# Kernel optimization log

Hardware: AMD Instinct MI355X
Metric: run time of the kernel (lower is better)

The kernel has to match this reference:

```python
import jax, jax.numpy as jnp
import numpy as np

LN_EPS = 1e-5
RMS_EPS = 1e-5

B, T, D = 4, 2048, 1024
H, DK, DV = 4, 256, 512            # head_k_dim = D/H, head_v_dim = expand_v * head_k_dim (expand_v=2)
KDIM, VDIM = H * DK, H * DV        # 1024, 2048
FFN = 4096                          # int(d_model * ffn_ratio)
CONV = 4


def _layernorm(x, w, b):
    mu = jnp.mean(x, -1, keepdims=True)
    var = jnp.mean(jnp.square(x - mu), -1, keepdims=True)
    return (x - mu) * jax.lax.rsqrt(var + LN_EPS) * w + b


def _short_conv_silu(x, w):
    # causal depthwise conv, kernel size K, then SiLU. x: [B,T,C], w: [C,K]
    K = w.shape[1]
    xp = jnp.pad(x, ((0, 0), (K - 1, 0), (0, 0)))
    y = sum(xp[:, i:i + x.shape[1], :] * w[:, i] for i in range(K))
    return jax.nn.silu(y)


def _l2norm(x):
    return x * jax.lax.rsqrt(jnp.sum(jnp.square(x), -1, keepdims=True) + 1e-6)


def _gated_delta_rule(q, k, v, g, beta):
    # q,k: [B,T,H,DK]; v: [B,T,H,DV]; g,beta: [B,T,H]
    # S_t = exp(g_t)*S_{t-1} + k_t (beta_t*(v_t - k_t^T exp(g_t) S_{t-1}))^T ; o_t = q_t^T S_t
    def step(S, inp):
        qt, kt, vt, gt, bt = inp
        S = S * jnp.exp(gt)[..., None, None]          # [B,H,DK,DV]
        mem = jnp.einsum('bhk,bhkv->bhv', kt, S)
        delta = (vt - mem) * bt[..., None]
        S = S + jnp.einsum('bhk,bhv->bhkv', kt, delta)
        o = jnp.einsum('bhk,bhkv->bhv', qt, S)
        return S, o
    S0 = jnp.zeros((q.shape[0], H, DK, DV), q.dtype)
    xs = (q.transpose(1, 0, 2, 3), k.transpose(1, 0, 2, 3), v.transpose(1, 0, 2, 3),
          g.transpose(1, 0, 2), beta.transpose(1, 0, 2))
    _, o = jax.lax.scan(step, S0, xs)
    return o.transpose(1, 0, 2, 3)  # [B,T,H,DV]


def setup_inputs() -> dict:
    key = jax.random.key(0)
    ks = jax.random.split(key, 24)
    n = lambda k, shp, s=0.02: jax.random.normal(k, shp, dtype=jnp.float32) * s
    return {
        'x': jax.random.normal(ks[0], (B, T, D), dtype=jnp.float32),
        'Wq': n(ks[1], (D, KDIM)), 'Wk': n(ks[2], (D, KDIM)), 'Wv': n(ks[3], (D, VDIM)),
        'Wa': n(ks[4], (D, H)), 'Wb': n(ks[5], (D, H)), 'Wg': n(ks[6], (D, VDIM)),
        'conv_q_w': n(ks[7], (KDIM, CONV), 0.2), 'conv_k_w': n(ks[8], (KDIM, CONV), 0.2),
        'conv_v_w': n(ks[9], (VDIM, CONV), 0.2),
        'A_log': jnp.log(jax.random.uniform(ks[10], (H,), minval=1.0, maxval=16.0, dtype=jnp.float32)),
        'dt_bias': jax.random.uniform(ks[11], (H,), minval=0.0, maxval=0.5, dtype=jnp.float32),
        'o_norm_w': jnp.ones((DV,), jnp.float32),
        'Wo': n(ks[12], (VDIM, D)),
        'ln1_w': jnp.ones((D,), jnp.float32), 'ln1_b': jnp.zeros((D,), jnp.float32),
        'ln2_w': jnp.ones((D,), jnp.float32), 'ln2_b': jnp.zeros((D,), jnp.float32),
        'ffn_w1': n(ks[13], (D, FFN)), 'ffn_b1': jnp.zeros((FFN,), jnp.float32),
        'ffn_w2': n(ks[14], (FFN, D)), 'ffn_b2': jnp.zeros((D,), jnp.float32),
    }


def reference(x, Wq, Wk, Wv, Wa, Wb, Wg, conv_q_w, conv_k_w, conv_v_w, A_log, dt_bias,
              o_norm_w, Wo, ln1_w, ln1_b, ln2_w, ln2_b, ffn_w1, ffn_b1, ffn_w2, ffn_b2):
    normed = _layernorm(x, ln1_w, ln1_b)
    q = _short_conv_silu(normed @ Wq, conv_q_w).reshape(B, T, H, DK)
    k = _short_conv_silu(normed @ Wk, conv_k_w).reshape(B, T, H, DK)
    v = _short_conv_silu(normed @ Wv, conv_v_w).reshape(B, T, H, DV)
    q = _l2norm(q) * (DK ** -0.5)
    k = _l2norm(k)
    g = -jnp.exp(A_log) * jax.nn.softplus(normed @ Wa + dt_bias)   # [B,T,H], negative
    beta = jax.nn.sigmoid(normed @ Wb)                              # [B,T,H]
    o = _gated_delta_rule(q, k, v, g, beta)                         # [B,T,H,DV]
    gate = (normed @ Wg).reshape(B, T, H, DV)
    o = o * jax.lax.rsqrt(jnp.mean(jnp.square(o), -1, keepdims=True) + RMS_EPS)
    o = o * o_norm_w * jax.nn.silu(gate)                            # gated RMSNorm
    x = x + o.reshape(B, T, VDIM) @ Wo
    h = _layernorm(x, ln2_w, ln2_b)
    ffn = jax.nn.gelu(h @ ffn_w1 + ffn_b1, approximate=False) @ ffn_w2 + ffn_b2
    return x + ffn
```

## Files before the change

kernel.cpp:

```cpp
#include <hip/hip_runtime.h>
#include <math.h>

#define B_    4
#define T_    2048
#define D_    1024
#define H_    4
#define DK_   256
#define DV_   512
#define KDIM_ 1024
#define VDIM_ 2048
#define FFN_  4096
#define BT_   8192

typedef unsigned short bf16;
typedef __attribute__((ext_vector_type(8))) short short8;
typedef __attribute__((ext_vector_type(4))) short short4v;
typedef __attribute__((ext_vector_type(4))) float f32x4;


__device__ __forceinline__ float sigmoidf_(float x) { return 1.f / (1.f + expf(-x)); }
__device__ __forceinline__ float siluf_(float x)    { return x / (1.f + expf(-x)); }
__device__ __forceinline__ float geluf_(float x)    { return 0.5f * x * (1.f + erff(x * 0.70710678118654752f)); }

__device__ __forceinline__ float bf2f(bf16 u) {
  union { unsigned int i; float f; } c; c.i = (unsigned int)u << 16; return c.f;
}
__device__ __forceinline__ bf16 f2bf(float f) {
  union { unsigned int i; float f; } c; c.f = f;
  unsigned int r = c.i + 0x7fffu + ((c.i >> 16) & 1u);
  return (bf16)(r >> 16);
}

__device__ __forceinline__ void gload16(const bf16* g, bf16* l) {
  __builtin_amdgcn_global_load_lds((__attribute__((address_space(1))) const void*)g,
                                   (__attribute__((address_space(3))) void*)l, 16, 0, 0);
}

__device__ __forceinline__ void storeC(float* p, float v) { *p = v; }
__device__ __forceinline__ void storeC(bf16* p, float v)  { *p = f2bf(v); }

__device__ __forceinline__ short8 ld76(const bf16* p) {
  union { short8 v; short4v h[2]; } u;
  u.h[0] = *(const short4v*)p;
  u.h[1] = *(const short4v*)(p + 4);
  return u.v;
}
__device__ __forceinline__ void st4bf(bf16* p, f32x4 v) {
  short4v o;
  o[0] = (short)f2bf(v[0]); o[1] = (short)f2bf(v[1]);
  o[2] = (short)f2bf(v[2]); o[3] = (short)f2bf(v[3]);
  *(short4v*)p = o;
}

__device__ __forceinline__ float block_sum256(float v, float* red) {
#pragma unroll
  for (int off = 32; off; off >>= 1) v += __shfl_xor(v, off, 64);
  __syncthreads();
  if ((threadIdx.x & 63) == 0) red[threadIdx.x >> 6] = v;
  __syncthreads();
  return red[0] + red[1] + red[2] + red[3];
}


__global__ __launch_bounds__(256) void sentinel_kernel(float* out, int n) {
  int i = blockIdx.x * 256 + threadIdx.x;
  if (i < n) out[i] = 12345.0f;
}


__global__ __launch_bounds__(256) void ln_kernel(const float* __restrict__ x,
                                                 const float* __restrict__ w,
                                                 const float* __restrict__ b,
                                                 bf16* __restrict__ y) {
  __shared__ float red[4];
  int row = blockIdx.x;
  const float* xr = x + (size_t)row * D_;
  float xv[4];
  float s = 0.f;
#pragma unroll
  for (int i = 0; i < 4; i++) { xv[i] = xr[threadIdx.x + 256 * i]; s += xv[i]; }
  float mean = block_sum256(s, red) * (1.f / D_);
  float s2 = 0.f;
#pragma unroll
  for (int i = 0; i < 4; i++) { float d = xv[i] - mean; s2 += d * d; }
  float var = block_sum256(s2, red) * (1.f / D_);
  float inv = rsqrtf(var + 1e-5f);
  bf16* yr = y + (size_t)row * D_;
#pragma unroll
  for (int i = 0; i < 4; i++) {
    int c = threadIdx.x + 256 * i;
    yr[c] = f2bf((xv[i] - mean) * inv * w[c] + b[c]);
  }
}


__global__ __launch_bounds__(256) void convT_kernel(const float* __restrict__ src,
                                                    bf16* __restrict__ dst,
                                                    int K, int N) {
  __shared__ float t[32][33];
  int n0 = blockIdx.x * 32, k0 = blockIdx.y * 32;
  int tx = threadIdx.x & 31, ty = threadIdx.x >> 5;
#pragma unroll
  for (int i = 0; i < 4; i++)
    t[ty + i * 8][tx] = src[(size_t)(k0 + ty + i * 8) * N + n0 + tx];
  __syncthreads();
#pragma unroll
  for (int i = 0; i < 4; i++)
    dst[(size_t)(n0 + ty + i * 8) * K + k0 + tx] = f2bf(t[tx][ty + i * 8]);
}


__global__ __launch_bounds__(256) void kT_kernel(const bf16* __restrict__ k16,
                                                 bf16* __restrict__ kT) {
  __shared__ bf16 tile[32][34];
  int t0 = blockIdx.x * 32;
  int d0 = blockIdx.y * 32;
  int bh = blockIdx.z;
  int b = bh >> 2, h = bh & 3;
  int tx = threadIdx.x & 31, ty = threadIdx.x >> 5;
#pragma unroll
  for (int i = 0; i < 4; i++)
    tile[ty + 8 * i][tx] = k16[(size_t)(b * T_ + t0 + ty + 8 * i) * KDIM_ + h * DK_ + d0 + tx];
  __syncthreads();
#pragma unroll
  for (int i = 0; i < 4; i++)
    kT[((size_t)bh * DK_ + d0 + ty + 8 * i) * T_ + t0 + tx] = tile[tx][ty + 8 * i];
}


template <typename TC>
__global__ __launch_bounds__(256) void gemm_mfma(const bf16* __restrict__ A,
                                                 const bf16* __restrict__ Bt,
                                                 const float* __restrict__ bias,
                                                 const float* __restrict__ res,
                                                 TC* __restrict__ C,
                                                 int N, int K, int flags) {
  __shared__ __align__(16) bf16 As[128 * 32];
  __shared__ __align__(16) bf16 Bs[128 * 32];
  int tid = threadIdx.x;
  int wave = tid >> 6, lane = tid & 63;
  int bm = blockIdx.y * 128, bn = blockIdx.x * 128;
  int wm = (wave >> 1) * 64, wn = (wave & 1) * 64;
  int lm = lane & 15;
  int quad = lane >> 4;

  f32x4 acc[4][4];
#pragma unroll
  for (int i = 0; i < 4; i++)
#pragma unroll
    for (int j = 0; j < 4; j++) acc[i][j] = (f32x4){0.f, 0.f, 0.f, 0.f};

  int srow = wave * 32 + (lane >> 2);
  int scol = (lane & 3) * 8;
  const bf16* ag = A  + (size_t)(bm + srow) * K + scol;
  const bf16* bg = Bt + (size_t)(bn + srow) * K + scol;
  bf16* al = As + wave * 32 * 32;
  bf16* bl = Bs + wave * 32 * 32;
  const size_t gstep = (size_t)16 * K;

  for (int k0 = 0; k0 < K; k0 += 32) {
    gload16(ag + k0,         al);
    gload16(ag + k0 + gstep, al + 16 * 32);
    gload16(bg + k0,         bl);
    gload16(bg + k0 + gstep, bl + 16 * 32);
    __syncthreads();

    short8 af[4], bf[4];
#pragma unroll
    for (int i = 0; i < 4; i++)
      af[i] = *(const short8*)&As[(wm + i * 16 + lm) * 32 + quad * 8];
#pragma unroll
    for (int j = 0; j < 4; j++)
      bf[j] = *(const short8*)&Bs[(wn + j * 16 + lm) * 32 + quad * 8];
#pragma unroll
    for (int i = 0; i < 4; i++)
#pragma unroll
      for (int j = 0; j < 4; j++)
        acc[i][j] = __builtin_amdgcn_mfma_f32_16x16x32_bf16(af[i], bf[j], acc[i][j], 0, 0, 0);
    __syncthreads();
  }

#pragma unroll
  for (int i = 0; i < 4; i++) {
    int row0 = bm + wm + i * 16 + quad * 4;
#pragma unroll
    for (int j = 0; j < 4; j++) {
      int col = bn + wn + j * 16 + lm;
      float badd = (flags & 1) ? bias[col] : 0.f;
#pragma unroll
      for (int r = 0; r < 4; r++) {
        float v = acc[i][j][r] + badd;
        if (flags & 2) v = geluf_(v);
        if (flags & 4) v += res[(size_t)(row0 + r) * N + col];
        storeC(&C[(size_t)(row0 + r) * N + col], v);
      }
    }
  }
}


__global__ __launch_bounds__(256) void ab_kernel(const bf16* __restrict__ normed,
                                                 const float* __restrict__ Wa,
                                                 const float* __restrict__ Wb,
                                                 const float* __restrict__ A_log,
                                                 const float* __restrict__ dt_bias,
                                                 float* __restrict__ g,
                                                 float* __restrict__ beta) {
  __shared__ float red[4];
  int row = blockIdx.x;
  const bf16* xr = normed + (size_t)row * D_;
  float aacc[4] = {}, bacc[4] = {};
#pragma unroll
  for (int i = 0; i < 4; i++) {
    int d = threadIdx.x + 256 * i;
    float xv = bf2f(xr[d]);
    float4 wa = *(const float4*)&Wa[d * 4];
    float4 wb = *(const float4*)&Wb[d * 4];
    aacc[0] += xv * wa.x; aacc[1] += xv * wa.y; aacc[2] += xv * wa.z; aacc[3] += xv * wa.w;
    bacc[0] += xv * wb.x; bacc[1] += xv * wb.y; bacc[2] += xv * wb.z; bacc[3] += xv * wb.w;
  }
  float sa[4], sb[4];
#pragma unroll
  for (int h = 0; h < 4; h++) {
    sa[h] = block_sum256(aacc[h], red);
    sb[h] = block_sum256(bacc[h], red);
  }
  if (threadIdx.x < 4) {
    int h = threadIdx.x;
    float xa = sa[h] + dt_bias[h];
    float sp = (xa > 20.f) ? xa : log1pf(expf(xa));
    g[row * 4 + h] = -expf(A_log[h]) * sp;
    beta[row * 4 + h] = sigmoidf_(sb[h]);
  }
}


__global__ __launch_bounds__(256) void conv_qk_kernel(const float* __restrict__ pre,
                                                      const float* __restrict__ convw,
                                                      bf16* __restrict__ out,
                                                      float scale) {
  __shared__ float red[4];
  int blk = blockIdx.x;
  int h = blk & 3;
  int bt = blk >> 2;
  int t = bt & (T_ - 1);
  int c = h * DK_ + threadIdx.x;
  float y = 0.f;
#pragma unroll
  for (int i = 0; i < 4; i++) {
    int tt = t + i - 3;
    if (tt >= 0) y += pre[(size_t)(bt + i - 3) * KDIM_ + c] * convw[c * 4 + i];
  }
  y = siluf_(y);
  float ss = block_sum256(y * y, red);
  y *= rsqrtf(ss + 1e-6f) * scale;
  out[(size_t)bt * KDIM_ + c] = f2bf(y);
}

__global__ __launch_bounds__(256) void conv_v_kernel(const float* __restrict__ pre,
                                                     const float* __restrict__ convw,
                                                     bf16* __restrict__ out) {
  int idx = blockIdx.x * 256 + threadIdx.x;
  int c = idx & (VDIM_ - 1);
  int bt = idx >> 11;
  int t = bt & (T_ - 1);
  float y = 0.f;
#pragma unroll
  for (int i = 0; i < 4; i++) {
    int tt = t + i - 3;
    if (tt >= 0) y += pre[(size_t)(bt + i - 3) * VDIM_ + c] * convw[c * 4 + i];
  }
  out[idx] = f2bf(siluf_(y));
}


#define SP 76

__global__ __launch_bounds__(256, 2) void delta_p1(const bf16* __restrict__ q,
                                                   const bf16* __restrict__ k,
                                                   const bf16* __restrict__ v,
                                                   const float* __restrict__ g,
                                                   const float* __restrict__ beta,
                                                   bf16* __restrict__ Pg,
                                                   bf16* __restrict__ Wg,
                                                   bf16* __restrict__ Yg,
                                                   float* __restrict__ gsc) {
  __shared__ bf16 Abf[64 * SP];
  __shared__ bf16 DTg[64 * SP];
  __shared__ float Ub[64 * 64];
  __shared__ float Gc[64], Lm[64], Bt[64];

  int blk = blockIdx.x;
  int c = blk & 31, bh = blk >> 5;
  int b = bh >> 2, h = bh & 3;
  int tid = threadIdx.x;
  int wave = tid >> 6, lane = tid & 63;
  int lm = lane & 15, quad = lane >> 4;
  int r0 = c * 64;

  const bf16* kb = k + (size_t)b * T_ * KDIM_ + h * DK_;
  const bf16* qb = q + (size_t)b * T_ * KDIM_ + h * DK_;
  const bf16* vb = v + (size_t)b * T_ * VDIM_ + h * DV_;
  const float* gbp = g    + (size_t)b * T_ * H_ + h;
  const float* bbp = beta + (size_t)b * T_ * H_ + h;
  size_t cb = (size_t)bh * 32 + c;
  bf16* PgC = Pg + cb * 4096;
  bf16* WgC = Wg + cb * 64 * 512;
  bf16* YgC = Yg + cb * 64 * 256;

  if (wave == 0) {
    float gv = gbp[(size_t)(r0 + lane) * H_];
    float bv = bbp[(size_t)(r0 + lane) * H_];
#pragma unroll
    for (int d = 1; d < 64; d <<= 1) {
      float nn = __shfl_up(gv, (unsigned)d, 64);
      if (lane >= d) gv += nn;
    }
    Gc[lane] = gv; Lm[lane] = expf(gv); Bt[lane] = bv;
    gsc[cb * 64 + lane] = gv;
  }
  __syncthreads();

  {
    f32x4 akk[4], aqk[4];
#pragma unroll
    for (int j = 0; j < 4; j++) { akk[j] = (f32x4){0.f,0.f,0.f,0.f}; aqk[j] = (f32x4){0.f,0.f,0.f,0.f}; }
    const bf16* krow = kb + (size_t)(r0 + 16 * wave + lm) * KDIM_;
    const bf16* qrow = qb + (size_t)(r0 + 16 * wave + lm) * KDIM_;
#pragma unroll
    for (int ks = 0; ks < 8; ks++) {
      short8 ak = *(const short8*)(krow + 8 * quad + 32 * ks);
      short8 aq = *(const short8*)(qrow + 8 * quad + 32 * ks);
#pragma unroll
      for (int j = 0; j < 4; j++) {
        short8 bk = *(const short8*)(kb + (size_t)(r0 + 16 * j + lm) * KDIM_ + 8 * quad + 32 * ks);
        akk[j] = __builtin_amdgcn_mfma_f32_16x16x32_bf16(ak, bk, akk[j], 0, 0, 0);
        aqk[j] = __builtin_amdgcn_mfma_f32_16x16x32_bf16(aq, bk, aqk[j], 0, 0, 0);
      }
    }
    float gi[4], bi[4];
#pragma unroll
    for (int r = 0; r < 4; r++) {
      int i = 16 * wave + 4 * quad + r;
      gi[r] = Gc[i]; bi[r] = Bt[i];
    }
#pragma unroll
    for (int j = 0; j < 4; j++) {
      int s = 16 * j + lm;
      float gs = Gc[s];
#pragma unroll
      for (int r = 0; r < 4; r++) {
        int i = 16 * wave + 4 * quad + r;
        float dec = expf(gi[r] - gs);
        Abf[(size_t)i * SP + s] = f2bf((s < i)  ? bi[r] * dec * akk[j][r] : 0.f);
        PgC[(size_t)i * 64 + s] = f2bf((s <= i) ? dec * aqk[j][r]        : 0.f);
      }
    }
  }

  for (int grp = 0; grp < 12; grp++) {
    __syncthreads();
    {
      int* dz = (int*)DTg;
#pragma unroll
      for (int i = 0; i < 10; i++) {
        int idx = tid + 256 * i;
        if (idx < 64 * SP / 2) dz[idx] = 0;
      }
    }
    int cg = 16 * wave + lm;
#pragma unroll
    for (int ti = 0; ti < 4; ti++)
#pragma unroll
      for (int r = 0; r < 4; r++) {
        int t = 16 * ti + 4 * quad + r;
        float val;
        if (grp < 8) val = Bt[t] * bf2f(vb[(size_t)(r0 + t) * VDIM_ + grp * 64 + cg]);
        else         val = Bt[t] * Lm[t] * bf2f(kb[(size_t)(r0 + t) * KDIM_ + (grp - 8) * 64 + cg]);
        Ub[t * 64 + cg] = val;
      }
    __syncthreads();

#pragma unroll
    for (int j = 0; j < 4; j++) {
      if (j > 0) {
        f32x4 racc = (f32x4){0.f, 0.f, 0.f, 0.f};
        int nk = (j == 3) ? 2 : 1;
        for (int ks = 0; ks < nk; ks++) {
          short8 aa = ld76(&Abf[(size_t)(16 * j + lm) * SP + 8 * quad + 32 * ks]);
          short8 bd = ld76(&DTg[(size_t)(16 * wave + lm) * SP + 8 * quad + 32 * ks]);
          racc = __builtin_amdgcn_mfma_f32_16x16x32_bf16(aa, bd, racc, 0, 0, 0);
        }
#pragma unroll
        for (int r = 0; r < 4; r++)
          Ub[(16 * j + 4 * quad + r) * 64 + 16 * wave + lm] -= racc[r];
        __syncthreads();
      }
      if (wave == 0) {
        int tl = lane & 15, sg = lane >> 4;
        short4v ab4 = *(const short4v*)&Abf[(size_t)(16 * j + tl) * SP + 16 * j + 4 * sg];
        float av[4];
        av[0] = bf2f((bf16)ab4[0]); av[1] = bf2f((bf16)ab4[1]);
        av[2] = bf2f((bf16)ab4[2]); av[3] = bf2f((bf16)ab4[3]);
        float d[16];
#pragma unroll
        for (int t = 0; t < 16; t++) {
          float val = Ub[(16 * j + t) * 64 + lane];
#pragma unroll
          for (int s = 0; s < t; s++) {
            float ats = __shfl(av[s & 3], t + 16 * (s >> 2), 64);
            val -= ats * d[s];
          }
          d[t] = val;
          DTg[(size_t)lane * SP + 16 * j + t] = f2bf(val);
        }
      }
      __syncthreads();
    }

#pragma unroll
    for (int ti = 0; ti < 4; ti++)
#pragma unroll
      for (int r = 0; r < 4; r++) {
        int t = 16 * ti + 4 * quad + r;
        bf16 val = DTg[(size_t)(16 * wave + lm) * SP + t];
        if (grp < 8) WgC[(size_t)t * 512 + grp * 64 + cg] = val;
        else         YgC[(size_t)t * 256 + (grp - 8) * 64 + cg] = val;
      }
  }
}


#define SP2 264
#define SD  72

__global__ __launch_bounds__(256, 1) void delta_p2(const bf16* __restrict__ q,
                                                   const bf16* __restrict__ kT,
                                                   const bf16* __restrict__ Wg,
                                                   const bf16* __restrict__ Yg,
                                                   const bf16* __restrict__ Pg,
                                                   const float* __restrict__ gsc,
                                                   bf16* __restrict__ o) {
  __shared__ bf16 ST[32 * SP2];
  __shared__ bf16 dT[32 * SD];
  __shared__ bf16 dTe[32 * SD];
  __shared__ float Gc[64];
  __shared__ __align__(16) bf16 Ks[8 * 256 * 8];

  int blk = blockIdx.x;
  int vs = blk & 15, bh = blk >> 4;
  int b = bh >> 2, h = bh & 3;
  int tid = threadIdx.x;
  int wave = tid >> 6, lane = tid & 63;
  int lm = lane & 15, quad = lane >> 4;
  int r2 = wave >> 1, ct = wave & 1;
  int v0 = vs * 32;

  const bf16* qb  = q  + (size_t)b * T_ * KDIM_ + h * DK_;
  const bf16* kTb = kT + (size_t)bh * DK_ * T_;
  bf16*       ob  = o  + (size_t)b * T_ * VDIM_ + h * DV_ + v0;

  f32x4 Sacc[8];
#pragma unroll
  for (int i = 0; i < 8; i++) Sacc[i] = (f32x4){0.f, 0.f, 0.f, 0.f};

  float gnext = gsc[(size_t)bh * 32 * 64 + lane];
  short8 qfr[2][8], yfr[2][8];
  {
    const bf16* yc0 = Yg + (size_t)bh * 32 * 64 * 256;
#pragma unroll
    for (int i = 0; i < 2; i++) {
      const bf16* qrow = qb + (size_t)(16 * (2 * r2 + i) + lm) * KDIM_;
      const bf16* yrow = yc0 + (size_t)(16 * (2 * r2 + i) + lm) * 256;
#pragma unroll
      for (int kf = 0; kf < 8; kf++) {
        qfr[i][kf] = *(const short8*)(qrow + 8 * quad + 32 * kf);
        yfr[i][kf] = *(const short8*)(yrow + 8 * quad + 32 * kf);
      }
    }
  }

  for (int c = 0; c < 32; c++) {
    const int r0 = c * 64;
    const size_t cb = (size_t)bh * 32 + c;

#pragma unroll
    for (int i = 0; i < 8; i++)
      gload16(kTb + (size_t)tid * T_ + r0 + i * 8, Ks + i * 2048 + wave * 512);
    __builtin_amdgcn_sched_barrier(0);

    const bf16* pc = Pg + cb * 4096;
    short8 pfr[2][2];
#pragma unroll
    for (int i = 0; i < 2; i++)
#pragma unroll
      for (int kf = 0; kf < 2; kf++)
        pfr[i][kf] = *(const short8*)(pc + (size_t)(16 * (2 * r2 + i) + lm) * 64 + 8 * quad + 32 * kf);

    const bf16* wcp = Wg + cb * 64 * 512 + v0 + 16 * ct + lm;
    bf16 wfr[2][4];
#pragma unroll
    for (int i = 0; i < 2; i++)
#pragma unroll
      for (int rr = 0; rr < 4; rr++)
        wfr[i][rr] = wcp[(size_t)(16 * (2 * r2 + i) + 4 * quad + rr) * 512];
    __builtin_amdgcn_sched_barrier(0);

#pragma unroll
    for (int di = 0; di < 8; di++)
      st4bf(&ST[(size_t)(16 * ct + lm) * SP2 + 16 * (8 * r2 + di) + 4 * quad], Sacc[di]);
    Gc[lane] = gnext;
    asm volatile("s_waitcnt lgkmcnt(0)" ::: "memory");
    __builtin_amdgcn_s_barrier();

    short8 Bs[8];
#pragma unroll
    for (int kf = 0; kf < 8; kf++)
      Bs[kf] = *(const short8*)&ST[(size_t)(16 * ct + lm) * SP2 + 8 * quad + 32 * kf];

    f32x4 Yacc[2], Oacc[2];
#pragma unroll
    for (int i = 0; i < 2; i++) { Yacc[i] = (f32x4){0.f,0.f,0.f,0.f}; Oacc[i] = (f32x4){0.f,0.f,0.f,0.f}; }
#pragma unroll
    for (int i = 0; i < 2; i++)
#pragma unroll
      for (int kf = 0; kf < 8; kf++) {
        Yacc[i] = __builtin_amdgcn_mfma_f32_16x16x32_bf16(yfr[i][kf], Bs[kf], Yacc[i], 0, 0, 0);
        Oacc[i] = __builtin_amdgcn_mfma_f32_16x16x32_bf16(qfr[i][kf], Bs[kf], Oacc[i], 0, 0, 0);
      }

    __builtin_amdgcn_sched_barrier(0);
    {
      int cn = (c + 1) & 31;
      size_t cbn = (size_t)bh * 32 + cn;
      int rn = cn * 64;
      gnext = gsc[cbn * 64 + lane];
      const bf16* ycn = Yg + cbn * 64 * 256;
#pragma unroll
      for (int i = 0; i < 2; i++) {
        const bf16* qrow = qb + (size_t)(rn + 16 * (2 * r2 + i) + lm) * KDIM_;
        const bf16* yrow = ycn + (size_t)(16 * (2 * r2 + i) + lm) * 256;
#pragma unroll
        for (int kf = 0; kf < 8; kf++) {
          qfr[i][kf] = *(const short8*)(qrow + 8 * quad + 32 * kf);
          yfr[i][kf] = *(const short8*)(yrow + 8 * quad + 32 * kf);
        }
      }
    }
    __builtin_amdgcn_sched_barrier(0);

    float g63 = Gc[63];
#pragma unroll
    for (int i = 0; i < 2; i++) {
      int rt = 2 * r2 + i;
#pragma unroll
      for (int rr = 0; rr < 4; rr++) {
        int row = 16 * rt + 4 * quad + rr;
        float gr  = Gc[row];
        float lam = expf(gr);
        float er  = expf(g63 - gr);
        float dv = bf2f(wfr[i][rr]) - Yacc[i][rr];
        Oacc[i][rr] *= lam;
        dT [(size_t)(16 * ct + lm) * SD + row] = f2bf(dv);
        dTe[(size_t)(16 * ct + lm) * SD + row] = f2bf(dv * er);
      }
    }
    asm volatile("s_waitcnt lgkmcnt(0)" ::: "memory");
    __builtin_amdgcn_s_barrier();

#pragma unroll
    for (int i = 0; i < 2; i++) {
#pragma unroll
      for (int kf = 0; kf < 2; kf++) {
        short8 bd = *(const short8*)&dT[(size_t)(16 * ct + lm) * SD + 8 * quad + 32 * kf];
        Oacc[i] = __builtin_amdgcn_mfma_f32_16x16x32_bf16(pfr[i][kf], bd, Oacc[i], 0, 0, 0);
      }
#pragma unroll
      for (int rr = 0; rr < 4; rr++) {
        int row = 16 * (2 * r2 + i) + 4 * quad + rr;
        ob[(size_t)(r0 + row) * VDIM_ + 16 * ct + lm] = f2bf(Oacc[i][rr]);
      }
    }

    float lend = expf(g63);
    short8 Be[2];
#pragma unroll
    for (int kf = 0; kf < 2; kf++)
      Be[kf] = *(const short8*)&dTe[(size_t)(16 * ct + lm) * SD + 8 * quad + 32 * kf];
#pragma unroll
    for (int di = 0; di < 8; di++) {
      int D = 8 * r2 + di;
      f32x4 s = Sacc[di];
      s[0] *= lend; s[1] *= lend; s[2] *= lend; s[3] *= lend;
#pragma unroll
      for (int kf = 0; kf < 2; kf++) {
        short8 ka = *(const short8*)&Ks[((size_t)(quad + 4 * kf) * 256 + 16 * D + lm) * 8];
        s = __builtin_amdgcn_mfma_f32_16x16x32_bf16(ka, Be[kf], s, 0, 0, 0);
      }
      Sacc[di] = s;
    }
    asm volatile("s_waitcnt lgkmcnt(0)" ::: "memory");
    __builtin_amdgcn_s_barrier();
  }
}


__global__ __launch_bounds__(256) void gated_rms_kernel(bf16* __restrict__ o,
                                                        const bf16* __restrict__ gate,
                                                        const float* __restrict__ onw) {
  __shared__ float red[4];
  int blk = blockIdx.x;
  int h = blk & 3;
  int bt = blk >> 2;
  size_t base = (size_t)bt * VDIM_ + h * DV_;
  int tid = threadIdx.x;
  float o1 = bf2f(o[base + tid]), o2 = bf2f(o[base + tid + 256]);
  float ss = block_sum256(o1 * o1 + o2 * o2, red);
  float s = rsqrtf(ss * (1.f / DV_) + 1e-5f);
  float g1 = bf2f(gate[base + tid]), g2 = bf2f(gate[base + tid + 256]);
  o[base + tid]       = f2bf(o1 * s * onw[tid] * siluf_(g1));
  o[base + tid + 256] = f2bf(o2 * s * onw[tid + 256] * siluf_(g2));
}


extern "C" void kernel_launch(void* const* d_in, const int* in_sizes, int n_in,
                              void* d_out, int out_size, void* d_ws, size_t ws_size,
                              hipStream_t stream) {
  const float* x        = (const float*)d_in[0];
  const float* Wq       = (const float*)d_in[1];
  const float* Wk       = (const float*)d_in[2];
  const float* Wv       = (const float*)d_in[3];
  const float* Wa       = (const float*)d_in[4];
  const float* Wb       = (const float*)d_in[5];
  const float* Wg       = (const float*)d_in[6];
  const float* conv_q_w = (const float*)d_in[7];
  const float* conv_k_w = (const float*)d_in[8];
  const float* conv_v_w = (const float*)d_in[9];
  const float* A_log    = (const float*)d_in[10];
  const float* dt_bias  = (const float*)d_in[11];
  const float* o_norm_w = (const float*)d_in[12];
  const float* Wo       = (const float*)d_in[13];
  const float* ln1_w    = (const float*)d_in[14];
  const float* ln1_b    = (const float*)d_in[15];
  const float* ln2_w    = (const float*)d_in[16];
  const float* ln2_b    = (const float*)d_in[17];
  const float* ffn_w1   = (const float*)d_in[18];
  const float* ffn_b1   = (const float*)d_in[19];
  const float* ffn_w2   = (const float*)d_in[20];
  const float* ffn_b2   = (const float*)d_in[21];

  size_t required = (size_t)218 << 20;
  if (ws_size < required) {
    sentinel_kernel<<<(out_size + 255) / 256, 256, 0, stream>>>((float*)d_out, out_size);
    return;
  }

  char* base = (char*)d_ws;
  float* pre    = (float*)(base);
  bf16*  normed = (bf16*)(base + ((size_t)64  << 20));
  bf16*  q16    = (bf16*)(base + ((size_t)80  << 20));
  bf16*  k16    = (bf16*)(base + ((size_t)96  << 20));
  bf16*  v16    = (bf16*)(base + ((size_t)112 << 20));
  bf16*  g16    = (bf16*)(base + ((size_t)144 << 20));
  bf16*  o16    = (bf16*)(base + ((size_t)176 << 20));
  bf16*  wslot  = (bf16*)(base + ((size_t)208 << 20));
  float* gvec   = (float*)(base + ((size_t)216 << 20));
  float* bvec   = gvec + (size_t)BT_ * H_;
  float* gsc    = (float*)(base + ((size_t)217 << 20));
  bf16*  Yg     = (bf16*)(base);
  bf16*  Wgb    = (bf16*)(base + ((size_t)16 << 20));
  bf16*  Pg     = (bf16*)(base + ((size_t)48 << 20));
  bf16*  kTg    = (bf16*)(base + ((size_t)52 << 20));
  float* x2     = (float*)(base);
  bf16*  hb16   = (bf16*)(base + ((size_t)64  << 20));
  bf16*  ffn1   = (bf16*)(base + ((size_t)80  << 20));

  ln_kernel<<<BT_, 256, 0, stream>>>(x, ln1_w, ln1_b, normed);

  convT_kernel<<<dim3(KDIM_ / 32, D_ / 32), 256, 0, stream>>>(Wq, wslot, D_, KDIM_);
  gemm_mfma<float><<<dim3(KDIM_ / 128, BT_ / 128), 256, 0, stream>>>(normed, wslot, nullptr, nullptr, pre, KDIM_, D_, 0);
  conv_qk_kernel<<<BT_ * H_, 256, 0, stream>>>(pre, conv_q_w, q16, 0.0625f);

  convT_kernel<<<dim3(KDIM_ / 32, D_ / 32), 256, 0, stream>>>(Wk, wslot, D_, KDIM_);
  gemm_mfma<float><<<dim3(KDIM_ / 128, BT_ / 128), 256, 0, stream>>>(normed, wslot, nullptr, nullptr, pre, KDIM_, D_, 0);
  conv_qk_kernel<<<BT_ * H_, 256, 0, stream>>>(pre, conv_k_w, k16, 1.0f);

  convT_kernel<<<dim3(VDIM_ / 32, D_ / 32), 256, 0, stream>>>(Wv, wslot, D_, VDIM_);
  gemm_mfma<float><<<dim3(VDIM_ / 128, BT_ / 128), 256, 0, stream>>>(normed, wslot, nullptr, nullptr, pre, VDIM_, D_, 0);
  conv_v_kernel<<<(BT_ * VDIM_) / 256, 256, 0, stream>>>(pre, conv_v_w, v16);

  convT_kernel<<<dim3(VDIM_ / 32, D_ / 32), 256, 0, stream>>>(Wg, wslot, D_, VDIM_);
  gemm_mfma<bf16><<<dim3(VDIM_ / 128, BT_ / 128), 256, 0, stream>>>(normed, wslot, nullptr, nullptr, g16, VDIM_, D_, 0);

  ab_kernel<<<BT_, 256, 0, stream>>>(normed, Wa, Wb, A_log, dt_bias, gvec, bvec);

  kT_kernel<<<dim3(T_ / 32, DK_ / 32, 16), 256, 0, stream>>>(k16, kTg);
  delta_p1<<<512, 256, 0, stream>>>(q16, k16, v16, gvec, bvec, Pg, Wgb, Yg, gsc);
  delta_p2<<<256, 256, 0, stream>>>(q16, kTg, Wgb, Yg, Pg, gsc, o16);

  gated_rms_kernel<<<BT_ * H_, 256, 0, stream>>>(o16, g16, o_norm_w);

  convT_kernel<<<dim3(D_ / 32, VDIM_ / 32), 256, 0, stream>>>(Wo, wslot, VDIM_, D_);
  gemm_mfma<float><<<dim3(D_ / 128, BT_ / 128), 256, 0, stream>>>(o16, wslot, nullptr, x, x2, D_, VDIM_, 4);

  ln_kernel<<<BT_, 256, 0, stream>>>(x2, ln2_w, ln2_b, hb16);

  convT_kernel<<<dim3(FFN_ / 32, D_ / 32), 256, 0, stream>>>(ffn_w1, wslot, D_, FFN_);
  gemm_mfma<bf16><<<dim3(FFN_ / 128, BT_ / 128), 256, 0, stream>>>(hb16, wslot, ffn_b1, nullptr, ffn1, FFN_, D_, 1 | 2);
  convT_kernel<<<dim3(D_ / 32, FFN_ / 32), 256, 0, stream>>>(ffn_w2, wslot, FFN_, D_);
  gemm_mfma<float><<<dim3(D_ / 128, BT_ / 128), 256, 0, stream>>>(ffn1, wslot, ffn_b2, x2, (float*)d_out, D_, FFN_, 1 | 4);
}
```

Before: 1.251 ms.

## Remap delta_p2 waves to row tiles and stage Wg chunk via LDS

Reassigns the four waves so that each wave owns one 16-row tile across both 16-column halves, instead of a 2x2 row/column split. This halves the per-wave q/y register fragments and the duplicated global q/Y loads. The Wg chunk is now loaded asynchronously into LDS alongside the key tile, replacing scattered scalar global loads. The delta writes to LDS are packed into 4-wide stores, fast __expf replaces expf, and the state update is reordered ahead of the output MFMA. In exchange each wave reads the full ST tile twice from LDS, and the fast exponential is slightly less accurate.

```diff
diff --git a/kernel.cpp b/kernel.cpp
--- a/kernel.cpp
+++ b/kernel.cpp
@@ -441,11 +441,12 @@
                                                    const bf16* __restrict__ Pg,
                                                    const float* __restrict__ gsc,
                                                    bf16* __restrict__ o) {
-  __shared__ bf16 ST[32 * SP2];
-  __shared__ bf16 dT[32 * SD];
-  __shared__ bf16 dTe[32 * SD];
+  __shared__ __align__(16) bf16 ST[32 * SP2];
+  __shared__ __align__(16) bf16 dT[32 * SD];
+  __shared__ __align__(16) bf16 dTe[32 * SD];
   __shared__ float Gc[64];
   __shared__ __align__(16) bf16 Ks[8 * 256 * 8];
+  __shared__ __align__(16) bf16 Ws[64 * 32];
 
   int blk = blockIdx.x;
   int vs = blk & 15, bh = blk >> 4;
@@ -453,30 +454,28 @@
   int tid = threadIdx.x;
   int wave = tid >> 6, lane = tid & 63;
   int lm = lane & 15, quad = lane >> 4;
-  int r2 = wave >> 1, ct = wave & 1;
+  int rt = wave;
   int v0 = vs * 32;
 
   const bf16* qb  = q  + (size_t)b * T_ * KDIM_ + h * DK_;
   const bf16* kTb = kT + (size_t)bh * DK_ * T_;
   bf16*       ob  = o  + (size_t)b * T_ * VDIM_ + h * DV_ + v0;
 
-  f32x4 Sacc[8];
-#pragma unroll
-  for (int i = 0; i < 8; i++) Sacc[i] = (f32x4){0.f, 0.f, 0.f, 0.f};
-
-  float gnext = gsc[(size_t)bh * 32 * 64 + lane];
-  short8 qfr[2][8], yfr[2][8];
+  f32x4 Sacc[4][2];
+#pragma unroll
+  for (int dd = 0; dd < 4; dd++)
+#pragma unroll
+    for (int cc = 0; cc < 2; cc++) Sacc[dd][cc] = (f32x4){0.f, 0.f, 0.f, 0.f};
+
+  float gnext = gsc[(size_t)bh * 2048 + lane];
+  short8 qfr[8], yfr[8];
   {
-    const bf16* yc0 = Yg + (size_t)bh * 32 * 64 * 256;
-#pragma unroll
-    for (int i = 0; i < 2; i++) {
-      const bf16* qrow = qb + (size_t)(16 * (2 * r2 + i) + lm) * KDIM_;
-      const bf16* yrow = yc0 + (size_t)(16 * (2 * r2 + i) + lm) * 256;
-#pragma unroll
-      for (int kf = 0; kf < 8; kf++) {
-        qfr[i][kf] = *(const short8*)(qrow + 8 * quad + 32 * kf);
-        yfr[i][kf] = *(const short8*)(yrow + 8 * quad + 32 * kf);
-      }
+    const bf16* qrow = qb + (size_t)(16 * rt + lm) * KDIM_;
+    const bf16* yrow = Yg + (size_t)bh * 32 * 16384 + (size_t)(16 * rt + lm) * 256;
+#pragma unroll
+    for (int kf = 0; kf < 8; kf++) {
+      qfr[kf] = *(const short8*)(qrow + 8 * quad + 32 * kf);
+      yfr[kf] = *(const short8*)(yrow + 8 * quad + 32 * kf);
     }
   }
 
@@ -487,117 +486,117 @@
 #pragma unroll
     for (int i = 0; i < 8; i++)
       gload16(kTb + (size_t)tid * T_ + r0 + i * 8, Ks + i * 2048 + wave * 512);
+    gload16(Wg + cb * 32768 + (size_t)(tid >> 2) * 512 + v0 + (tid & 3) * 8, Ws + tid * 8);
     __builtin_amdgcn_sched_barrier(0);
 
-    const bf16* pc = Pg + cb * 4096;
-    short8 pfr[2][2];
-#pragma unroll
-    for (int i = 0; i < 2; i++)
-#pragma unroll
-      for (int kf = 0; kf < 2; kf++)
-        pfr[i][kf] = *(const short8*)(pc + (size_t)(16 * (2 * r2 + i) + lm) * 64 + 8 * quad + 32 * kf);
-
-    const bf16* wcp = Wg + cb * 64 * 512 + v0 + 16 * ct + lm;
-    bf16 wfr[2][4];
-#pragma unroll
-    for (int i = 0; i < 2; i++)
-#pragma unroll
-      for (int rr = 0; rr < 4; rr++)
-        wfr[i][rr] = wcp[(size_t)(16 * (2 * r2 + i) + 4 * quad + rr) * 512];
+    const bf16* pc = Pg + cb * 4096 + (size_t)(16 * rt + lm) * 64 + 8 * quad;
+    short8 pfr[2];
+    pfr[0] = *(const short8*)(pc);
+    pfr[1] = *(const short8*)(pc + 32);
     __builtin_amdgcn_sched_barrier(0);
 
 #pragma unroll
-    for (int di = 0; di < 8; di++)
-      st4bf(&ST[(size_t)(16 * ct + lm) * SP2 + 16 * (8 * r2 + di) + 4 * quad], Sacc[di]);
+    for (int dd = 0; dd < 4; dd++)
+#pragma unroll
+      for (int cc = 0; cc < 2; cc++)
+        st4bf(&ST[(size_t)(16 * cc + lm) * SP2 + 16 * (4 * wave + dd) + 4 * quad], Sacc[dd][cc]);
     Gc[lane] = gnext;
     asm volatile("s_waitcnt lgkmcnt(0)" ::: "memory");
     __builtin_amdgcn_s_barrier();
 
-    short8 Bs[8];
-#pragma unroll
-    for (int kf = 0; kf < 8; kf++)
-      Bs[kf] = *(const short8*)&ST[(size_t)(16 * ct + lm) * SP2 + 8 * quad + 32 * kf];
-
     f32x4 Yacc[2], Oacc[2];
 #pragma unroll
-    for (int i = 0; i < 2; i++) { Yacc[i] = (f32x4){0.f,0.f,0.f,0.f}; Oacc[i] = (f32x4){0.f,0.f,0.f,0.f}; }
-#pragma unroll
-    for (int i = 0; i < 2; i++)
+    for (int cc = 0; cc < 2; cc++) { Yacc[cc] = (f32x4){0.f,0.f,0.f,0.f}; Oacc[cc] = (f32x4){0.f,0.f,0.f,0.f}; }
+#pragma unroll
+    for (int cc = 0; cc < 2; cc++) {
+      short8 Bs[8];
+#pragma unroll
+      for (int kf = 0; kf < 8; kf++)
+        Bs[kf] = *(const short8*)&ST[(size_t)(16 * cc + lm) * SP2 + 8 * quad + 32 * kf];
 #pragma unroll
       for (int kf = 0; kf < 8; kf++) {
-        Yacc[i] = __builtin_amdgcn_mfma_f32_16x16x32_bf16(yfr[i][kf], Bs[kf], Yacc[i], 0, 0, 0);
-        Oacc[i] = __builtin_amdgcn_mfma_f32_16x16x32_bf16(qfr[i][kf], Bs[kf], Oacc[i], 0, 0, 0);
-      }
-
+        Yacc[cc] = __builtin_amdgcn_mfma_f32_16x16x32_bf16(yfr[kf], Bs[kf], Yacc[cc], 0, 0, 0);
+        Oacc[cc] = __builtin_amdgcn_mfma_f32_16x16x32_bf16(qfr[kf], Bs[kf], Oacc[cc], 0, 0, 0);
+      }
+    }
     __builtin_amdgcn_sched_barrier(0);
+
     {
       int cn = (c + 1) & 31;
       size_t cbn = (size_t)bh * 32 + cn;
-      int rn = cn * 64;
       gnext = gsc[cbn * 64 + lane];
-      const bf16* ycn = Yg + cbn * 64 * 256;
-#pragma unroll
-      for (int i = 0; i < 2; i++) {
-        const bf16* qrow = qb + (size_t)(rn + 16 * (2 * r2 + i) + lm) * KDIM_;
-        const bf16* yrow = ycn + (size_t)(16 * (2 * r2 + i) + lm) * 256;
-#pragma unroll
-        for (int kf = 0; kf < 8; kf++) {
-          qfr[i][kf] = *(const short8*)(qrow + 8 * quad + 32 * kf);
-          yfr[i][kf] = *(const short8*)(yrow + 8 * quad + 32 * kf);
-        }
+      const bf16* qrow = qb + (size_t)(cn * 64 + 16 * rt + lm) * KDIM_;
+      const bf16* yrow = Yg + cbn * 16384 + (size_t)(16 * rt + lm) * 256;
+#pragma unroll
+      for (int kf = 0; kf < 8; kf++) {
+        qfr[kf] = *(const short8*)(qrow + 8 * quad + 32 * kf);
+        yfr[kf] = *(const short8*)(yrow + 8 * quad + 32 * kf);
       }
     }
     __builtin_amdgcn_sched_barrier(0);
 
+    asm volatile("" : : "v"(*(const int*)&pfr[0]), "v"(*(const int*)&pfr[1]) : "memory");
+    __builtin_amdgcn_sched_barrier(0);
     float g63 = Gc[63];
-#pragma unroll
-    for (int i = 0; i < 2; i++) {
-      int rt = 2 * r2 + i;
+    float lamv[4], erv[4];
+#pragma unroll
+    for (int rr = 0; rr < 4; rr++) {
+      float gr = Gc[16 * rt + 4 * quad + rr];
+      lamv[rr] = __expf(gr);
+      erv[rr]  = __expf(g63 - gr);
+    }
+#pragma unroll
+    for (int cc = 0; cc < 2; cc++) {
+      short4v dpack, depack;
 #pragma unroll
       for (int rr = 0; rr < 4; rr++) {
         int row = 16 * rt + 4 * quad + rr;
-        float gr  = Gc[row];
-        float lam = expf(gr);
-        float er  = expf(g63 - gr);
-        float dv = bf2f(wfr[i][rr]) - Yacc[i][rr];
-        Oacc[i][rr] *= lam;
-        dT [(size_t)(16 * ct + lm) * SD + row] = f2bf(dv);
-        dTe[(size_t)(16 * ct + lm) * SD + row] = f2bf(dv * er);
-      }
+        float dv = bf2f(Ws[row * 32 + 16 * cc + lm]) - Yacc[cc][rr];
+        Oacc[cc][rr] *= lamv[rr];
+        dpack[rr]  = (short)f2bf(dv);
+        depack[rr] = (short)f2bf(dv * erv[rr]);
+      }
+      *(short4v*)&dT [(size_t)(16 * cc + lm) * SD + 16 * rt + 4 * quad] = dpack;
+      *(short4v*)&dTe[(size_t)(16 * cc + lm) * SD + 16 * rt + 4 * quad] = depack;
     }
     asm volatile("s_waitcnt lgkmcnt(0)" ::: "memory");
     __builtin_amdgcn_s_barrier();
 
-#pragma unroll
-    for (int i = 0; i < 2; i++) {
+    float lend = __expf(g63);
+    short8 Be[2][2];
+#pragma unroll
+    for (int cc = 0; cc < 2; cc++)
+#pragma unroll
+      for (int kf = 0; kf < 2; kf++)
+        Be[cc][kf] = ld76(&dTe[(size_t)(16 * cc + lm) * SD + 8 * quad + 32 * kf]);
+#pragma unroll
+    for (int dd = 0; dd < 4; dd++) {
+      int Dt = 4 * wave + dd;
+#pragma unroll
+      for (int cc = 0; cc < 2; cc++) {
+        f32x4 s = Sacc[dd][cc];
+        s[0] *= lend; s[1] *= lend; s[2] *= lend; s[3] *= lend;
+#pragma unroll
+        for (int kf = 0; kf < 2; kf++) {
+          short8 ka = *(const short8*)&Ks[((size_t)(quad + 4 * kf) * 256 + 16 * Dt + lm) * 8];
+          s = __builtin_amdgcn_mfma_f32_16x16x32_bf16(ka, Be[cc][kf], s, 0, 0, 0);
+        }
+        Sacc[dd][cc] = s;
+      }
+    }
+
+#pragma unroll
+    for (int cc = 0; cc < 2; cc++) {
 #pragma unroll
       for (int kf = 0; kf < 2; kf++) {
-        short8 bd = *(const short8*)&dT[(size_t)(16 * ct + lm) * SD + 8 * quad + 32 * kf];
-        Oacc[i] = __builtin_amdgcn_mfma_f32_16x16x32_bf16(pfr[i][kf], bd, Oacc[i], 0, 0, 0);
+        short8 bd = ld76(&dT[(size_t)(16 * cc + lm) * SD + 8 * quad + 32 * kf]);
+        Oacc[cc] = __builtin_amdgcn_mfma_f32_16x16x32_bf16(pfr[kf], bd, Oacc[cc], 0, 0, 0);
       }
 #pragma unroll
       for (int rr = 0; rr < 4; rr++) {
-        int row = 16 * (2 * r2 + i) + 4 * quad + rr;
-        ob[(size_t)(r0 + row) * VDIM_ + 16 * ct + lm] = f2bf(Oacc[i][rr]);
-      }
-    }
-
-    float lend = expf(g63);
-    short8 Be[2];
-#pragma unroll
-    for (int kf = 0; kf < 2; kf++)
-      Be[kf] = *(const short8*)&dTe[(size_t)(16 * ct + lm) * SD + 8 * quad + 32 * kf];
-#pragma unroll
-    for (int di = 0; di < 8; di++) {
-      int D = 8 * r2 + di;
-      f32x4 s = Sacc[di];
-      s[0] *= lend; s[1] *= lend; s[2] *= lend; s[3] *= lend;
-#pragma unroll
-      for (int kf = 0; kf < 2; kf++) {
-        short8 ka = *(const short8*)&Ks[((size_t)(quad + 4 * kf) * 256 + 16 * D + lm) * 8];
-        s = __builtin_amdgcn_mfma_f32_16x16x32_bf16(ka, Be[kf], s, 0, 0, 0);
-      }
-      Sacc[di] = s;
+        int row = 16 * rt + 4 * quad + rr;
+        ob[(size_t)(r0 + row) * VDIM_ + 16 * cc + lm] = f2bf(Oacc[cc][rr]);
+      }
     }
     asm volatile("s_waitcnt lgkmcnt(0)" ::: "memory");
     __builtin_amdgcn_s_barrier();
```

After: 1.187 ms. 5.1% less time.
